# Kernel optimization log

Measured on AMD Instinct MI355X. Metric: run time of the kernel, lower is better.

## Reference

```python
import jax, jax.numpy as jnp
import numpy as np

D_MODEL = 1024
N_HEADS = 16
HEAD_DIM = D_MODEL // N_HEADS


def rotate_half(x):
    # interleaved rotate: (-x_odd, x_even) re-interleaved
    x1 = x[..., ::2]
    x2 = x[..., 1::2]
    return jnp.stack((-x2, x1), axis=-1).reshape(x.shape)


def rope_tables(seq_len, dim, dtype):
    inv_freq = 1.0 / (10000.0 ** (jnp.arange(0, dim, 2, dtype=jnp.float32) / dim))
    t = jnp.arange(seq_len, dtype=jnp.float32)
    freqs = jnp.einsum('i,j->ij', t, inv_freq)          # [T, dim/2]
    emb = jnp.concatenate((freqs, freqs), axis=-1)       # [T, dim]
    return jnp.cos(emb).astype(dtype)[None, None], jnp.sin(emb).astype(dtype)[None, None]


def setup_inputs() -> dict:
    key = jax.random.key(0)
    k1, k2, k3 = jax.random.split(key, 3)
    B, T, C = 2, 2048, D_MODEL
    scale_in = 1.0 / np.sqrt(C)
    return {
        'x': jax.random.normal(k1, (B, T, C), dtype=jnp.float32),
        'attention_mask': jnp.ones((B, T), dtype=jnp.int32),
        'qkv_w': jax.random.normal(k2, (3 * C, C), dtype=jnp.float32) * scale_in,
        'qkv_b': jnp.zeros((3 * C,), dtype=jnp.float32),
        'out_w': jax.random.normal(k3, (C, C), dtype=jnp.float32) * scale_in,
        'out_b': jnp.zeros((C,), dtype=jnp.float32),
    }


def reference(x, attention_mask, qkv_w, qkv_b, out_w, out_b):
    B, T, C = x.shape
    H, Dh = N_HEADS, HEAD_DIM
    qkv = x @ qkv_w.T + qkv_b                             # [B,T,3C]
    q, k, v = jnp.split(qkv, 3, axis=-1)
    q = q.reshape(B, T, H, Dh).transpose(0, 2, 1, 3)      # [B,H,T,Dh]
    k = k.reshape(B, T, H, Dh).transpose(0, 2, 1, 3)
    v = v.reshape(B, T, H, Dh).transpose(0, 2, 1, 3)
    cos, sin = rope_tables(T, Dh, x.dtype)                # [1,1,T,Dh]
    q = q * cos + rotate_half(q) * sin
    k = k * cos + rotate_half(k) * sin
    att = jnp.einsum('bhqd,bhkd->bhqk', q, k) / jnp.sqrt(jnp.array(Dh, x.dtype))
    causal = jnp.tril(jnp.ones((T, T), dtype=bool))[None, None]
    key_mask = attention_mask.astype(bool)[:, None, None, :]
    neg_inf = jnp.array(-jnp.inf, att.dtype)
    att = jnp.where(causal & key_mask, att, neg_inf)
    att = jax.nn.softmax(att, axis=-1)
    query_mask = attention_mask.astype(bool)[:, None, :, None]
    att = att * query_mask
    y = jnp.einsum('bhqk,bhkd->bhqd', att, v)             # [B,H,T,Dh]
    y = y.transpose(0, 2, 1, 3).reshape(B, T, C)
    y = y * attention_mask[:, :, None].astype(y.dtype)
    y = y @ out_w.T + out_b
    return y
```

## Files before the change

### kernel.cpp

```cpp
#include <hip/hip_runtime.h>
#include <hip/hip_bf16.h>

typedef __bf16 bf16;
typedef __bf16 bf16x4 __attribute__((ext_vector_type(4)));
typedef __bf16 bf16x8 __attribute__((ext_vector_type(8)));
typedef float f32x4 __attribute__((ext_vector_type(4)));
typedef unsigned int u32x4 __attribute__((ext_vector_type(4)));

#define T_LEN 2048
#define NHEAD 16
#define DHEAD 64
#define CDIM 1024
#define NB 2

__device__ __forceinline__ void g2l16(const void* g, void* l) {
    __builtin_amdgcn_global_load_lds(
        (const __attribute__((address_space(1))) unsigned int*)g,
        (__attribute__((address_space(3))) unsigned int*)l, 16, 0, 0);
}

__device__ __forceinline__ float fexp2(float x) {
    float r;
    asm("v_exp_f32 %0, %1" : "=v"(r) : "v"(x));
    return r;
}

__device__ __forceinline__ void stage_swz256(const bf16* __restrict__ g, size_t gstride,
                                             bf16* lds, int t) {
#pragma unroll
    for (int c = 0; c < 2; c++) {
        int off = c * 4096 + t * 16;
        int row = off >> 7;
        int lcol = (off & 127) ^ ((row & 7) << 4);
        g2l16(g + (size_t)row * gstride + (lcol >> 1), (char*)lds + off);
    }
}

__device__ __forceinline__ bf16x8 rd_swz(const bf16* lds, int row, int colB) {
    return *(const bf16x8*)((const char*)lds + row * 128 + (colB ^ ((row & 7) << 4)));
}

__global__ __launch_bounds__(256) void prep_kernel(
    const float* __restrict__ x, const float* __restrict__ qkv_w,
    const float* __restrict__ out_w, const int* __restrict__ am,
    bf16* __restrict__ xb, bf16* __restrict__ wqb, bf16* __restrict__ wob,
    float* __restrict__ ct, float* __restrict__ st, float* __restrict__ mf,
    int* __restrict__ mflag) {
    int bid = blockIdx.x;
    if (bid < 4096) {
        int i = bid * 256 + threadIdx.x;
        const float* src; bf16* dst; int j;
        if (i < 524288)      { src = x;     dst = xb;  j = i; }
        else if (i < 917504) { src = qkv_w; dst = wqb; j = i - 524288; }
        else                 { src = out_w; dst = wob; j = i - 917504; }
        const float4* p = (const float4*)src + (size_t)j * 2;
        float4 a = p[0], b = p[1];
        bf16x8 o;
        o[0] = (bf16)a.x; o[1] = (bf16)a.y; o[2] = (bf16)a.z; o[3] = (bf16)a.w;
        o[4] = (bf16)b.x; o[5] = (bf16)b.y; o[6] = (bf16)b.z; o[7] = (bf16)b.w;
        ((bf16x8*)dst)[j] = o;
    } else if (bid < 4608) {
        int i = (bid - 4096) * 256 + threadIdx.x;
        int t = i >> 6, d = i & 63;
        float ex = (float)(2 * (d & 31)) / 64.0f;
        float inv = powf(10000.0f, -ex);
        float ang = (float)t * inv;
        ct[i] = cosf(ang);
        st[i] = sinf(ang);
    } else {
        int i = (bid - 4608) * 256 + threadIdx.x;
        int v = am[i];
        mf[i] = (v != 0) ? 0.0f : -1e30f;
        unsigned long long bz = __ballot(v == 0);
        if ((threadIdx.x & 63) == 0) mflag[i >> 6] = (bz != 0) ? 1 : 0;
    }
}

__global__ __launch_bounds__(512, 4) void gemm_qkv_kernel(
    const bf16* __restrict__ xb, const bf16* __restrict__ wb,
    const float* __restrict__ bias,
    const float* __restrict__ ct, const float* __restrict__ st,
    bf16* __restrict__ qg, bf16* __restrict__ kg, bf16* __restrict__ vt) {
    __shared__ __align__(16) bf16 smem[2][2 * 128 * 64];
    int m0 = blockIdx.x * 128, n0 = blockIdx.y * 128;
    int t = threadIdx.x, w = t >> 6, l = t & 63;
    int wm = w & 3, wn = w >> 2;
    int l15 = l & 15, lhi = l >> 4;
    f32x4 acc[2][4] = {};
#pragma unroll
    for (int c = 0; c < 2; c++) {
        int off = c * 8192 + t * 16;
        int row = off >> 7;
        int lcol = (off & 127) ^ ((row & 7) << 4);
        g2l16(xb + (size_t)(m0 + row) * CDIM + (lcol >> 1), (char*)smem[0] + off);
        g2l16(wb + (size_t)(n0 + row) * CDIM + (lcol >> 1), (char*)(smem[0] + 128 * 64) + off);
    }
    __syncthreads();
    int cur = 0;
    for (int k0 = 0; k0 < CDIM; k0 += 64) {
        if (k0 + 64 < CDIM) {
#pragma unroll
            for (int c = 0; c < 2; c++) {
                int off = c * 8192 + t * 16;
                int row = off >> 7;
                int lcol = (off & 127) ^ ((row & 7) << 4);
                g2l16(xb + (size_t)(m0 + row) * CDIM + k0 + 64 + (lcol >> 1),
                      (char*)smem[cur ^ 1] + off);
                g2l16(wb + (size_t)(n0 + row) * CDIM + k0 + 64 + (lcol >> 1),
                      (char*)(smem[cur ^ 1] + 128 * 64) + off);
            }
        }
        bf16* sA = smem[cur];
        bf16* sB = smem[cur] + 128 * 64;
#pragma unroll
        for (int ks = 0; ks < 2; ks++) {
            bf16x8 af[2], bfr[4];
#pragma unroll
            for (int mt = 0; mt < 2; mt++)
                af[mt] = rd_swz(sA, wm * 32 + mt * 16 + l15, ks * 64 + lhi * 16);
#pragma unroll
            for (int nt = 0; nt < 4; nt++)
                bfr[nt] = rd_swz(sB, wn * 64 + nt * 16 + l15, ks * 64 + lhi * 16);
#pragma unroll
            for (int mt = 0; mt < 2; mt++)
#pragma unroll
                for (int nt = 0; nt < 4; nt++)
                    acc[mt][nt] = __builtin_amdgcn_mfma_f32_16x16x32_bf16(
                        af[mt], bfr[nt], acc[mt][nt], 0, 0, 0);
        }
        __syncthreads();
        cur ^= 1;
    }
    int bb = m0 >> 11, tt0 = m0 & 2047;
    if (n0 >= 2048) {
        bf16* sT = (bf16*)smem;
#pragma unroll
        for (int pass = 0; pass < 2; pass++) {
            __syncthreads();
            if (wn == pass) {
#pragma unroll
                for (int nt = 0; nt < 4; nt++) {
                    int dl = nt * 16 + l15;
                    float cb = bias[n0 + pass * 64 + dl];
#pragma unroll
                    for (int mt = 0; mt < 2; mt++) {
                        bf16x4 pv;
#pragma unroll
                        for (int r = 0; r < 4; r++) pv[r] = (bf16)(acc[mt][nt][r] + cb);
                        *(bf16x4*)(sT + dl * 136 + wm * 32 + mt * 16 + lhi * 4) = pv;
                    }
                }
            }
            __syncthreads();
            int h_p = ((n0 & 1023) >> 6) + pass;
            size_t vbase = ((size_t)(bb * NHEAD + h_p)) * T_LEN * DHEAD + tt0;
#pragma unroll
            for (int c = 0; c < 2; c++) {
                int cid = c * 512 + t;
                int d = cid >> 4, ch = cid & 15;
                *(bf16x8*)(vt + vbase + (size_t)d * T_LEN + ch * 8) =
                    *(const bf16x8*)(sT + d * 136 + ch * 8);
            }
        }
        return;
    }
    int sec = n0 >> 10;
    bf16* og = (sec == 0) ? qg : kg;
    float oscale = (sec == 0) ? 0.125f * 1.44269504f : 1.0f;
#pragma unroll
    for (int nt = 0; nt < 4; nt++) {
        int col = n0 + wn * 64 + nt * 16 + l15;
        int cc = col & 1023;
        int h = cc >> 6, d = cc & 63;
        float cb = bias[col];
        size_t hb = ((size_t)(bb * NHEAD + h)) * T_LEN * DHEAD;
#pragma unroll
        for (int mt = 0; mt < 2; mt++) {
#pragma unroll
            for (int r = 0; r < 4; r++) {
                int tt = tt0 + wm * 32 + mt * 16 + lhi * 4 + r;
                float v = acc[mt][nt][r] + cb;
                float p = __shfl_xor(v, 1);
                float cs = ct[tt * 64 + d], sn = st[tt * 64 + d];
                float o = (d & 1) ? (v * cs + p * sn) : (v * cs - p * sn);
                og[hb + (size_t)tt * DHEAD + d] = (bf16)(o * oscale);
            }
        }
    }
}

__global__ __launch_bounds__(256, 4) void attn_kernel(
    const bf16* __restrict__ qg, const bf16* __restrict__ kg, const bf16* __restrict__ vt,
    const float* __restrict__ maskf, const int* __restrict__ mflag,
    bf16* __restrict__ yb) {
    __shared__ __align__(16) bf16 sK[2][64 * 64];
    __shared__ __align__(16) bf16 sV[2][64 * 64];
    int lin = blockIdx.x;
    int xcd = lin & 7, idx = lin >> 3;
    int group = idx >> 4, pos = idx & 15;
    int pair = xcd * 4 + group;
    int h = pair & 15, b = pair >> 4;
    int t = threadIdx.x, w = t >> 6, l = t & 63;
    int l15 = l & 15, lhi = l >> 4;
    const size_t head_off = ((size_t)(b * NHEAD + h)) * T_LEN * DHEAD;
    const bf16* qb = qg + head_off;
    const bf16* kb = kg + head_off;
    const bf16* vb = vt + head_off;
    const float* mrow = maskf + b * T_LEN;
    const int* mfl = mflag + b * (T_LEN / 64);
    const u32x4 onesu = {0x3F803F80u, 0x3F803F80u, 0x3F803F80u, 0x3F803F80u};
    const bf16x8 ones8 = __builtin_bit_cast(bf16x8, onesu);
    stage_swz256(kb, DHEAD, sK[0], t);
    stage_swz256(vb, T_LEN, sV[0], t);
#pragma unroll 1
    for (int ph = 0; ph < 2; ph++) {
        int qt = ph ? (31 - pos) : pos;
        int q0 = qt * 64;
        const int wq0 = q0 + w * 16;
        const int qrow_l = wq0 + l15;
        bf16x8 qf[2];
        qf[0] = *(const bf16x8*)(qb + (size_t)qrow_l * DHEAD + lhi * 8);
        qf[1] = *(const bf16x8*)(qb + (size_t)qrow_l * DHEAD + 32 + lhi * 8);
        f32x4 lsv = {};
        f32x4 accy[4] = {};
        __syncthreads();
        int cur = 0;
        for (int kv0 = 0; kv0 <= q0; kv0 += 64) {
            if (kv0 + 64 <= q0) {
                stage_swz256(kb + (size_t)(kv0 + 64) * DHEAD, DHEAD, sK[cur ^ 1], t);
                stage_swz256(vb + (kv0 + 64), T_LEN, sV[cur ^ 1], t);
            }
            if (kv0 <= wq0 + 15) {
                f32x4 s[4] = {};
                __builtin_amdgcn_s_setprio(1);
#pragma unroll
                for (int c = 0; c < 4; c++)
#pragma unroll
                    for (int ks = 0; ks < 2; ks++) {
                        bf16x8 kf = rd_swz(sK[cur], c * 16 + l15, ks * 64 + lhi * 16);
                        s[c] = __builtin_amdgcn_mfma_f32_16x16x32_bf16(kf, qf[ks], s[c], 0, 0, 0);
                    }
                __builtin_amdgcn_s_setprio(0);
                bool diag = (kv0 + 63 > wq0);
                int needmask = mfl[kv0 >> 6];
                if (needmask || diag) {
#pragma unroll
                    for (int c = 0; c < 4; c++) {
                        float mpv[4] = {0.f, 0.f, 0.f, 0.f};
                        if (needmask) {
                            float4 mq = *(const float4*)(mrow + kv0 + c * 16 + lhi * 4);
                            mpv[0] = mq.x; mpv[1] = mq.y; mpv[2] = mq.z; mpv[3] = mq.w;
                        }
#pragma unroll
                        for (int r = 0; r < 4; r++) {
                            float sv = s[c][r] + mpv[r];
                            if (diag && (kv0 + c * 16 + lhi * 4 + r > qrow_l)) sv = -1e30f;
                            s[c][r] = sv;
                        }
                    }
                }
#pragma unroll
                for (int c = 0; c < 4; c++)
#pragma unroll
                    for (int r = 0; r < 4; r++) s[c][r] = fexp2(s[c][r]);
                __builtin_amdgcn_s_setprio(1);
#pragma unroll
                for (int g2 = 0; g2 < 2; g2++) {
                    unsigned a0, a1, b0, b1;
                    asm("v_cvt_pk_bf16_f32 %0, %1, %2" : "=v"(a0) : "v"(s[2 * g2][0]), "v"(s[2 * g2][1]));
                    asm("v_cvt_pk_bf16_f32 %0, %1, %2" : "=v"(a1) : "v"(s[2 * g2][2]), "v"(s[2 * g2][3]));
                    asm("v_cvt_pk_bf16_f32 %0, %1, %2" : "=v"(b0) : "v"(s[2 * g2 + 1][0]), "v"(s[2 * g2 + 1][1]));
                    asm("v_cvt_pk_bf16_f32 %0, %1, %2" : "=v"(b1) : "v"(s[2 * g2 + 1][2]), "v"(s[2 * g2 + 1][3]));
                    asm("v_permlane32_swap_b32 %0, %1" : "+v"(a0), "+v"(b0));
                    asm("v_permlane16_swap_b32 %0, %1" : "+v"(a0), "+v"(b0));
                    asm("v_permlane32_swap_b32 %0, %1" : "+v"(a1), "+v"(b1));
                    asm("v_permlane16_swap_b32 %0, %1" : "+v"(a1), "+v"(b1));
                    u32x4 pu;
                    pu[0] = a0; pu[1] = a1; pu[2] = b0; pu[3] = b1;
                    bf16x8 pv = __builtin_bit_cast(bf16x8, pu);
                    lsv = __builtin_amdgcn_mfma_f32_16x16x32_bf16(pv, ones8, lsv, 0, 0, 0);
#pragma unroll
                    for (int dt = 0; dt < 4; dt++) {
                        bf16x8 vf = rd_swz(sV[cur], dt * 16 + l15, g2 * 64 + lhi * 16);
                        accy[dt] = __builtin_amdgcn_mfma_f32_16x16x32_bf16(pv, vf, accy[dt], 0, 0, 0);
                    }
                }
                __builtin_amdgcn_s_setprio(0);
            }
            __syncthreads();
            cur ^= 1;
        }
        if (ph == 0) {
            stage_swz256(kb, DHEAD, sK[0], t);
            stage_swz256(vb, T_LEN, sV[0], t);
        }
#pragma unroll
        for (int r = 0; r < 4; r++) {
            float inv = lsv[r] > 0.f ? 1.0f / lsv[r] : 0.0f;
            int rowt = wq0 + lhi * 4 + r;
            size_t obase = ((size_t)(b * T_LEN + rowt)) * CDIM + (size_t)h * DHEAD;
#pragma unroll
            for (int dt = 0; dt < 4; dt++)
                yb[obase + dt * 16 + l15] = (bf16)(accy[dt][r] * inv);
        }
    }
}

__global__ __launch_bounds__(256) void gemm_out_kernel(
    const bf16* __restrict__ yb, const bf16* __restrict__ wb,
    const float* __restrict__ bias, float* __restrict__ out) {
    __shared__ __align__(16) bf16 smem[2][128 * 64 + 64 * 64];
    int m0 = blockIdx.x * 128, n0 = blockIdx.y * 64;
    int t = threadIdx.x, w = t >> 6, l = t & 63;
    int wm = w >> 1, wn = w & 1;
    int l15 = l & 15, lhi = l >> 4;
    f32x4 acc[4][2] = {};
#pragma unroll
    for (int i = 0; i < 4; i++) {
        int off = i * 4096 + t * 16;
        int row = off >> 7;
        int lcol = (off & 127) ^ ((row & 7) << 4);
        g2l16(yb + (size_t)(m0 + row) * CDIM + (lcol >> 1), (char*)smem[0] + off);
        if (i < 2)
            g2l16(wb + (size_t)(n0 + row) * CDIM + (lcol >> 1),
                  (char*)(smem[0] + 128 * 64) + off);
    }
    __syncthreads();
    int cur = 0;
    for (int k0 = 0; k0 < CDIM; k0 += 64) {
        if (k0 + 64 < CDIM) {
#pragma unroll
            for (int i = 0; i < 4; i++) {
                int off = i * 4096 + t * 16;
                int row = off >> 7;
                int lcol = (off & 127) ^ ((row & 7) << 4);
                g2l16(yb + (size_t)(m0 + row) * CDIM + k0 + 64 + (lcol >> 1),
                      (char*)smem[cur ^ 1] + off);
                if (i < 2)
                    g2l16(wb + (size_t)(n0 + row) * CDIM + k0 + 64 + (lcol >> 1),
                          (char*)(smem[cur ^ 1] + 128 * 64) + off);
            }
        }
        bf16* sA = smem[cur];
        bf16* sB = smem[cur] + 128 * 64;
#pragma unroll
        for (int ks = 0; ks < 2; ks++) {
            bf16x8 af[4], bfr[2];
#pragma unroll
            for (int mt = 0; mt < 4; mt++)
                af[mt] = rd_swz(sA, wm * 64 + mt * 16 + l15, ks * 64 + lhi * 16);
#pragma unroll
            for (int nt = 0; nt < 2; nt++)
                bfr[nt] = rd_swz(sB, wn * 32 + nt * 16 + l15, ks * 64 + lhi * 16);
#pragma unroll
            for (int mt = 0; mt < 4; mt++)
#pragma unroll
                for (int nt = 0; nt < 2; nt++)
                    acc[mt][nt] = __builtin_amdgcn_mfma_f32_16x16x32_bf16(
                        af[mt], bfr[nt], acc[mt][nt], 0, 0, 0);
        }
        __syncthreads();
        cur ^= 1;
    }
#pragma unroll
    for (int nt = 0; nt < 2; nt++) {
        int col = n0 + wn * 32 + nt * 16 + l15;
        float cb = bias[col];
#pragma unroll
        for (int mt = 0; mt < 4; mt++) {
#pragma unroll
            for (int r = 0; r < 4; r++) {
                int rowm = m0 + wm * 64 + mt * 16 + lhi * 4 + r;
                out[(size_t)rowm * CDIM + col] = acc[mt][nt][r] + cb;
            }
        }
    }
}

extern "C" void kernel_launch(void* const* d_in, const int* in_sizes, int n_in,
                              void* d_out, int out_size, void* d_ws, size_t ws_size,
                              hipStream_t stream) {
    const float* x      = (const float*)d_in[0];
    const int*   amask  = (const int*)d_in[1];
    const float* qkv_w  = (const float*)d_in[2];
    const float* qkv_b  = (const float*)d_in[3];
    const float* out_w  = (const float*)d_in[4];
    const float* out_b  = (const float*)d_in[5];
    float* out = (float*)d_out;

    char* ws = (char*)d_ws;
    bf16* xb  = (bf16*)(ws);
    bf16* wqb = (bf16*)(ws + (8ull  << 20));
    bf16* wob = (bf16*)(ws + (14ull << 20));
    bf16* qg  = (bf16*)(ws + (16ull << 20));
    bf16* kg  = (bf16*)(ws + (24ull << 20));
    bf16* vt  = (bf16*)(ws + (32ull << 20));
    bf16* yb  = (bf16*)(ws + (40ull << 20));
    float* ctab = (float*)(ws + (48ull << 20));
    float* stab = (float*)(ws + (48ull << 20) + (1ull << 19));
    float* mkf  = (float*)(ws + (49ull << 20));
    int*   mfg  = (int*)(ws + (49ull << 20) + (16ull << 10));

    prep_kernel<<<4624, 256, 0, stream>>>(x, qkv_w, out_w, amask,
                                          xb, wqb, wob, ctab, stab, mkf, mfg);
    gemm_qkv_kernel<<<dim3(32, 24), 512, 0, stream>>>(xb, wqb, qkv_b, ctab, stab, qg, kg, vt);
    attn_kernel<<<dim3(512), 256, 0, stream>>>(qg, kg, vt, mkf, mfg, yb);
    gemm_out_kernel<<<dim3(32, 16), 256, 0, stream>>>(yb, wob, out_b, out);
}
```

Before: 96.29 us.

## Switch attention to 32x32x16 MFMA with 128-row query tiles

Reworks the attention kernel so each wave handles 32 query rows using 32x32x16 bf16 MFMA instead of 16x16x32, and each block processes 128-row query tiles. The grid is halved to 256 blocks and the occupancy hint drops to 2 blocks per CU. The larger MFMA tile raises operand reuse per LDS read and removes a permlane16 swap per P fragment. In exchange there is less parallelism (256 blocks on 256 CUs), heavier register use, and extra causal tail iterations per tile.

```diff
diff --git a/kernel.cpp b/kernel.cpp
--- a/kernel.cpp
+++ b/kernel.cpp
@@ -5,6 +5,7 @@
 typedef __bf16 bf16x4 __attribute__((ext_vector_type(4)));
 typedef __bf16 bf16x8 __attribute__((ext_vector_type(8)));
 typedef float f32x4 __attribute__((ext_vector_type(4)));
+typedef float f32x16 __attribute__((ext_vector_type(16)));
 typedef unsigned int u32x4 __attribute__((ext_vector_type(4)));
 
 #define T_LEN 2048
@@ -189,7 +190,7 @@
     }
 }
 
-__global__ __launch_bounds__(256, 4) void attn_kernel(
+__global__ __launch_bounds__(256, 2) void attn_kernel(
     const bf16* __restrict__ qg, const bf16* __restrict__ kg, const bf16* __restrict__ vt,
     const float* __restrict__ maskf, const int* __restrict__ mflag,
     bf16* __restrict__ yb) {
@@ -197,11 +198,11 @@
     __shared__ __align__(16) bf16 sV[2][64 * 64];
     int lin = blockIdx.x;
     int xcd = lin & 7, idx = lin >> 3;
-    int group = idx >> 4, pos = idx & 15;
+    int group = idx >> 3, pos = idx & 7;
     int pair = xcd * 4 + group;
     int h = pair & 15, b = pair >> 4;
     int t = threadIdx.x, w = t >> 6, l = t & 63;
-    int l15 = l & 15, lhi = l >> 4;
+    int l31 = l & 31, lg = l >> 5;
     const size_t head_off = ((size_t)(b * NHEAD + h)) * T_LEN * DHEAD;
     const bf16* qb = qg + head_off;
     const bf16* kb = kg + head_off;
@@ -214,75 +215,79 @@
     stage_swz256(vb, T_LEN, sV[0], t);
 #pragma unroll 1
     for (int ph = 0; ph < 2; ph++) {
-        int qt = ph ? (31 - pos) : pos;
-        int q0 = qt * 64;
-        const int wq0 = q0 + w * 16;
-        const int qrow_l = wq0 + l15;
-        bf16x8 qf[2];
-        qf[0] = *(const bf16x8*)(qb + (size_t)qrow_l * DHEAD + lhi * 8);
-        qf[1] = *(const bf16x8*)(qb + (size_t)qrow_l * DHEAD + 32 + lhi * 8);
-        f32x4 lsv = {};
-        f32x4 accy[4] = {};
+        int qt = ph ? (15 - pos) : pos;
+        int q0 = qt * 128;
+        const int wq0 = q0 + w * 32;
+        const int qrow_l = wq0 + l31;
+        bf16x8 qf[4];
+#pragma unroll
+        for (int ks = 0; ks < 4; ks++)
+            qf[ks] = *(const bf16x8*)(qb + (size_t)qrow_l * DHEAD + ks * 16 + lg * 8);
+        f32x16 lsv = {};
+        f32x16 accy[2] = {};
         __syncthreads();
         int cur = 0;
-        for (int kv0 = 0; kv0 <= q0; kv0 += 64) {
-            if (kv0 + 64 <= q0) {
+        const int kv_end = q0 + 64;
+        for (int kv0 = 0; kv0 <= kv_end; kv0 += 64) {
+            if (kv0 + 64 <= kv_end) {
                 stage_swz256(kb + (size_t)(kv0 + 64) * DHEAD, DHEAD, sK[cur ^ 1], t);
                 stage_swz256(vb + (kv0 + 64), T_LEN, sV[cur ^ 1], t);
             }
-            if (kv0 <= wq0 + 15) {
-                f32x4 s[4] = {};
+            if (kv0 <= wq0 + 31) {
+                f32x16 s[2] = {};
                 __builtin_amdgcn_s_setprio(1);
 #pragma unroll
-                for (int c = 0; c < 4; c++)
-#pragma unroll
-                    for (int ks = 0; ks < 2; ks++) {
-                        bf16x8 kf = rd_swz(sK[cur], c * 16 + l15, ks * 64 + lhi * 16);
-                        s[c] = __builtin_amdgcn_mfma_f32_16x16x32_bf16(kf, qf[ks], s[c], 0, 0, 0);
+                for (int ct = 0; ct < 2; ct++)
+#pragma unroll
+                    for (int ks = 0; ks < 4; ks++) {
+                        bf16x8 kf = rd_swz(sK[cur], ct * 32 + l31, ks * 32 + lg * 16);
+                        s[ct] = __builtin_amdgcn_mfma_f32_32x32x16_bf16(kf, qf[ks], s[ct], 0, 0, 0);
                     }
                 __builtin_amdgcn_s_setprio(0);
                 bool diag = (kv0 + 63 > wq0);
                 int needmask = mfl[kv0 >> 6];
                 if (needmask || diag) {
 #pragma unroll
-                    for (int c = 0; c < 4; c++) {
-                        float mpv[4] = {0.f, 0.f, 0.f, 0.f};
-                        if (needmask) {
-                            float4 mq = *(const float4*)(mrow + kv0 + c * 16 + lhi * 4);
-                            mpv[0] = mq.x; mpv[1] = mq.y; mpv[2] = mq.z; mpv[3] = mq.w;
+                    for (int ctm = 0; ctm < 2; ctm++)
+#pragma unroll
+                        for (int g = 0; g < 4; g++) {
+                            float mpv[4] = {0.f, 0.f, 0.f, 0.f};
+                            if (needmask) {
+                                float4 mq = *(const float4*)(mrow + kv0 + ctm * 32 + 8 * g + 4 * lg);
+                                mpv[0] = mq.x; mpv[1] = mq.y; mpv[2] = mq.z; mpv[3] = mq.w;
+                            }
+#pragma unroll
+                            for (int r2 = 0; r2 < 4; r2++) {
+                                int kvv = kv0 + ctm * 32 + 8 * g + 4 * lg + r2;
+                                float sv = s[ctm][g * 4 + r2] + mpv[r2];
+                                if (diag && (kvv > qrow_l)) sv = -1e30f;
+                                s[ctm][g * 4 + r2] = sv;
+                            }
                         }
-#pragma unroll
-                        for (int r = 0; r < 4; r++) {
-                            float sv = s[c][r] + mpv[r];
-                            if (diag && (kv0 + c * 16 + lhi * 4 + r > qrow_l)) sv = -1e30f;
-                            s[c][r] = sv;
-                        }
-                    }
                 }
 #pragma unroll
-                for (int c = 0; c < 4; c++)
-#pragma unroll
-                    for (int r = 0; r < 4; r++) s[c][r] = fexp2(s[c][r]);
+                for (int ctm = 0; ctm < 2; ctm++)
+#pragma unroll
+                    for (int r = 0; r < 16; r++) s[ctm][r] = fexp2(s[ctm][r]);
                 __builtin_amdgcn_s_setprio(1);
 #pragma unroll
-                for (int g2 = 0; g2 < 2; g2++) {
+                for (int m = 0; m < 4; m++) {
+                    int ctm = m >> 1, rb = (m & 1) * 8;
                     unsigned a0, a1, b0, b1;
-                    asm("v_cvt_pk_bf16_f32 %0, %1, %2" : "=v"(a0) : "v"(s[2 * g2][0]), "v"(s[2 * g2][1]));
-                    asm("v_cvt_pk_bf16_f32 %0, %1, %2" : "=v"(a1) : "v"(s[2 * g2][2]), "v"(s[2 * g2][3]));
-                    asm("v_cvt_pk_bf16_f32 %0, %1, %2" : "=v"(b0) : "v"(s[2 * g2 + 1][0]), "v"(s[2 * g2 + 1][1]));
-                    asm("v_cvt_pk_bf16_f32 %0, %1, %2" : "=v"(b1) : "v"(s[2 * g2 + 1][2]), "v"(s[2 * g2 + 1][3]));
+                    asm("v_cvt_pk_bf16_f32 %0, %1, %2" : "=v"(a0) : "v"(s[ctm][rb + 0]), "v"(s[ctm][rb + 1]));
+                    asm("v_cvt_pk_bf16_f32 %0, %1, %2" : "=v"(a1) : "v"(s[ctm][rb + 2]), "v"(s[ctm][rb + 3]));
+                    asm("v_cvt_pk_bf16_f32 %0, %1, %2" : "=v"(b0) : "v"(s[ctm][rb + 4]), "v"(s[ctm][rb + 5]));
+                    asm("v_cvt_pk_bf16_f32 %0, %1, %2" : "=v"(b1) : "v"(s[ctm][rb + 6]), "v"(s[ctm][rb + 7]));
                     asm("v_permlane32_swap_b32 %0, %1" : "+v"(a0), "+v"(b0));
-                    asm("v_permlane16_swap_b32 %0, %1" : "+v"(a0), "+v"(b0));
                     asm("v_permlane32_swap_b32 %0, %1" : "+v"(a1), "+v"(b1));
-                    asm("v_permlane16_swap_b32 %0, %1" : "+v"(a1), "+v"(b1));
                     u32x4 pu;
                     pu[0] = a0; pu[1] = a1; pu[2] = b0; pu[3] = b1;
                     bf16x8 pv = __builtin_bit_cast(bf16x8, pu);
-                    lsv = __builtin_amdgcn_mfma_f32_16x16x32_bf16(pv, ones8, lsv, 0, 0, 0);
-#pragma unroll
-                    for (int dt = 0; dt < 4; dt++) {
-                        bf16x8 vf = rd_swz(sV[cur], dt * 16 + l15, g2 * 64 + lhi * 16);
-                        accy[dt] = __builtin_amdgcn_mfma_f32_16x16x32_bf16(pv, vf, accy[dt], 0, 0, 0);
+                    lsv = __builtin_amdgcn_mfma_f32_32x32x16_bf16(pv, ones8, lsv, 0, 0, 0);
+#pragma unroll
+                    for (int dt = 0; dt < 2; dt++) {
+                        bf16x8 vf = rd_swz(sV[cur], dt * 32 + l31, m * 32 + lg * 16);
+                        accy[dt] = __builtin_amdgcn_mfma_f32_32x32x16_bf16(pv, vf, accy[dt], 0, 0, 0);
                     }
                 }
                 __builtin_amdgcn_s_setprio(0);
@@ -295,13 +300,13 @@
             stage_swz256(vb, T_LEN, sV[0], t);
         }
 #pragma unroll
-        for (int r = 0; r < 4; r++) {
+        for (int r = 0; r < 16; r++) {
             float inv = lsv[r] > 0.f ? 1.0f / lsv[r] : 0.0f;
-            int rowt = wq0 + lhi * 4 + r;
+            int rowt = wq0 + (r & 3) + 8 * (r >> 2) + 4 * lg;
             size_t obase = ((size_t)(b * T_LEN + rowt)) * CDIM + (size_t)h * DHEAD;
 #pragma unroll
-            for (int dt = 0; dt < 4; dt++)
-                yb[obase + dt * 16 + l15] = (bf16)(accy[dt][r] * inv);
+            for (int dt = 0; dt < 2; dt++)
+                yb[obase + dt * 32 + l31] = (bf16)(accy[dt][r] * inv);
         }
     }
 }
@@ -404,6 +409,6 @@
     prep_kernel<<<4624, 256, 0, stream>>>(x, qkv_w, out_w, amask,
                                           xb, wqb, wob, ctab, stab, mkf, mfg);
     gemm_qkv_kernel<<<dim3(32, 24), 512, 0, stream>>>(xb, wqb, qkv_b, ctab, stab, qg, kg, vt);
-    attn_kernel<<<dim3(512), 256, 0, stream>>>(qg, kg, vt, mkf, mfg, yb);
+    attn_kernel<<<dim3(256), 256, 0, stream>>>(qg, kg, vt, mkf, mfg, yb);
     gemm_out_kernel<<<dim3(32, 16), 256, 0, stream>>>(yb, wob, out_b, out);
 }
```

After: 101.4 us. +5.3%, slower.
